# Kernel optimization log

Hardware: AMD Instinct MI355X
Metric: run time of the kernel (lower is better)

## Reference

```python
import jax, jax.numpy as jnp
import numpy as np

TOP_K = 2
B, S, H, I, E = 1, 2048, 1024, 4096, 8


def setup_inputs() -> dict:
    key = jax.random.key(0)
    k1, k2, k3, k4 = jax.random.split(key, 4)
    x = jax.random.normal(k1, (B, S, H), dtype=jnp.float32)
    gate_w = jax.random.normal(k2, (E, H), dtype=jnp.float32)
    w1 = jax.random.normal(k3, (E, I, H), dtype=jnp.float32)
    w2 = jax.random.normal(k4, (E, H, I), dtype=jnp.float32)
    return {"x": x, "gate_w": gate_w, "w1": w1, "w2": w2}


def reference(x, gate_w, w1, w2):
    b, s, h = x.shape
    xf = x.reshape(-1, h)                      # [T, H]
    T = xf.shape[0]
    logits = xf @ gate_w.T                     # [T, E]
    probs = jax.nn.softmax(logits, axis=-1)
    wts, idx = jax.lax.top_k(probs, TOP_K)     # [T, k]
    wts = wts / jnp.sum(wts, axis=-1, keepdims=True)
    # combine[t, e] = routing weight of expert e for token t (0 if not selected)
    combine = jnp.zeros((T, w1.shape[0]), dtype=x.dtype)
    combine = combine.at[jnp.arange(T)[:, None], idx].add(wts)
    # dense dispatch: every expert processes every token, masked/weighted by combine
    hid = jax.nn.silu(jnp.einsum('th,eih->tei', xf, w1))   # [T, E, I]
    y = jnp.einsum('tei,ehi->teh', hid, w2)                # [T, E, H]
    out = jnp.einsum('teh,te->th', y, combine)             # [T, H]
    return out.reshape(b, s, h)
```

## Files before the change

### kernel.cpp

```cpp
#include <hip/hip_runtime.h>
#include <stdint.h>

#define TT 2048
#define HH 1024
#define II 4096
#define EE 8
#define KS 4

typedef __attribute__((ext_vector_type(4))) float floatx4;
typedef __attribute__((ext_vector_type(8))) __bf16 bf16x8;

__device__ __forceinline__ unsigned short f2bf(float f) {
  union { float f; unsigned u; } v; v.f = f;
  return (unsigned short)((v.u + 0x7FFFu + ((v.u >> 16) & 1u)) >> 16);
}

__device__ __forceinline__ void async_ld16(const void* g, void* l) {
  __builtin_amdgcn_global_load_lds(
      (__attribute__((address_space(1))) void*)g,
      (__attribute__((address_space(3))) void*)l, 16, 0, 0);
}

__global__ __launch_bounds__(256) void k_gating(
    const float* __restrict__ x, const float* __restrict__ gw,
    unsigned short* __restrict__ xb, int* __restrict__ sel_e,
    float* __restrict__ sel_w, int* __restrict__ counts) {
  int t = blockIdx.x;
  int tid = threadIdx.x;
  floatx4 xv = ((const floatx4*)(x + (size_t)t * HH))[tid];
  ushort4 xo;
  xo.x = f2bf(xv.x); xo.y = f2bf(xv.y); xo.z = f2bf(xv.z); xo.w = f2bf(xv.w);
  ((ushort4*)(xb + (size_t)t * HH))[tid] = xo;

  float part[EE];
#pragma unroll
  for (int e = 0; e < EE; e++) {
    floatx4 g = ((const floatx4*)(gw + e * HH))[tid];
    part[e] = xv.x * g.x + xv.y * g.y + xv.z * g.z + xv.w * g.w;
  }
#pragma unroll
  for (int e = 0; e < EE; e++) {
    float v = part[e];
#pragma unroll
    for (int off = 32; off > 0; off >>= 1) v += __shfl_down(v, off, 64);
    part[e] = v;
  }
  __shared__ float red[4][EE];
  int wave = tid >> 6;
  if ((tid & 63) == 0) {
#pragma unroll
    for (int e = 0; e < EE; e++) red[wave][e] = part[e];
  }
  __syncthreads();
  if (tid == 0) {
    float lg[EE];
#pragma unroll
    for (int e = 0; e < EE; e++)
      lg[e] = red[0][e] + red[1][e] + red[2][e] + red[3][e];
    int e0 = 0;
#pragma unroll
    for (int e = 1; e < EE; e++) if (lg[e] > lg[e0]) e0 = e;
    int e1 = (e0 == 0) ? 1 : 0;
#pragma unroll
    for (int e = 0; e < EE; e++) if (e != e0 && lg[e] > lg[e1]) e1 = e;
    float w0 = 1.f / (1.f + expf(lg[e1] - lg[e0]));
    sel_e[t * 2] = e0; sel_e[t * 2 + 1] = e1;
    sel_w[t * 2] = w0; sel_w[t * 2 + 1] = 1.f - w0;
    atomicAdd(&counts[e0], 1);
    atomicAdd(&counts[e1], 1);
  }
}

__global__ __launch_bounds__(256) void k_fill(
    const int* __restrict__ counts, const int* __restrict__ sel_e,
    const float* __restrict__ sel_w, int* __restrict__ bases,
    int* __restrict__ row_token, float* __restrict__ row_w,
    int* __restrict__ inv_slot) {
  __shared__ int lb[EE];
  __shared__ int lc[EE];
  int tid = threadIdx.x;
  if (tid == 0) {
    int s = 0;
    for (int e = 0; e < EE; e++) { lb[e] = s; s += counts[e]; }
  }
  if (tid < EE) lc[tid] = 0;
  __syncthreads();
  for (int p = tid; p < TT * 2; p += 256) {
    int e = sel_e[p];
    int slot = lb[e] + atomicAdd(&lc[e], 1);
    row_token[slot] = p >> 1;
    row_w[slot] = sel_w[p];
    inv_slot[p] = slot;
  }
  __syncthreads();
  if (tid < EE) bases[tid] = lb[tid];
}

__global__ __launch_bounds__(256) void k_gemm1(
    const unsigned short* __restrict__ xb,
    const float* __restrict__ w1,
    unsigned short* __restrict__ hid,
    const int* __restrict__ counts, const int* __restrict__ bases,
    const int* __restrict__ row_token) {
  const int e = blockIdx.z;
  const int count = counts[e];
  const int m0 = blockIdx.y * 128;
  if (m0 >= count) return;
  const int n0 = blockIdx.x * 128;
  const int base = bases[e];

  __shared__ __align__(16) unsigned short Smem[128 * 32 * 2];
  unsigned short* As = Smem;
  unsigned short* Bs = Smem + 128 * 32;

  const int tid = threadIdx.x;
  const int lane = tid & 63;
  const int wave = tid >> 6;
  const int wm = (wave & 1) * 64;
  const int wn = (wave >> 1) * 64;
  const int quad = lane >> 4;
  const int l16 = lane & 15;

  const int rA0 = tid >> 2;
  const int rA1 = rA0 + 64;
  const int cc = (tid & 3) * 8;

  int g0 = m0 + rA0; if (g0 > count - 1) g0 = count - 1;
  int g1 = m0 + rA1; if (g1 > count - 1) g1 = count - 1;
  const unsigned short* aS0 = xb + (size_t)row_token[base + g0] * HH + cc;
  const unsigned short* aS1 = xb + (size_t)row_token[base + g1] * HH + cc;
  const float* wp = w1 + (size_t)e * II * HH;
  const float* bp0 = wp + (size_t)(n0 + rA0) * HH + cc;
  const float* bp1 = wp + (size_t)(n0 + rA1) * HH + cc;

  unsigned short* lA0 = As + tid * 8;
  unsigned short* lA1 = As + tid * 8 + 2048;
  unsigned short* lB0 = Bs + tid * 8;
  unsigned short* lB1 = Bs + tid * 8 + 2048;

  const floatx4 fz = {0.f, 0.f, 0.f, 0.f};
  floatx4 acc[4][4];
#pragma unroll
  for (int i = 0; i < 4; i++)
#pragma unroll
    for (int j = 0; j < 4; j++) acc[i][j] = fz;

  floatx4 f0a = *(const floatx4*)(bp0);
  floatx4 f0b = *(const floatx4*)(bp0 + 4);
  floatx4 f1a = *(const floatx4*)(bp1);
  floatx4 f1b = *(const floatx4*)(bp1 + 4);

  for (int k0 = 0; k0 < HH; k0 += 32) {
    bf16x8 wv0, wv1;
#pragma unroll
    for (int j = 0; j < 4; j++) {
      wv0[j] = (__bf16)f0a[j]; wv0[j + 4] = (__bf16)f0b[j];
      wv1[j] = (__bf16)f1a[j]; wv1[j + 4] = (__bf16)f1b[j];
    }
    *(bf16x8*)lB0 = wv0;
    *(bf16x8*)lB1 = wv1;
    async_ld16(aS0 + k0, lA0);
    async_ld16(aS1 + k0, lA1);
    __syncthreads();
    if (k0 + 32 < HH) {
      f0a = *(const floatx4*)(bp0 + k0 + 32);
      f0b = *(const floatx4*)(bp0 + k0 + 36);
      f1a = *(const floatx4*)(bp1 + k0 + 32);
      f1b = *(const floatx4*)(bp1 + k0 + 36);
    }
    bf16x8 af[4], bfr[4];
#pragma unroll
    for (int i = 0; i < 4; i++) {
      af[i]  = *(const bf16x8*)(As + (wm + i * 16 + l16) * 32 + quad * 8);
      bfr[i] = *(const bf16x8*)(Bs + (wn + i * 16 + l16) * 32 + quad * 8);
    }
#pragma unroll
    for (int i = 0; i < 4; i++)
#pragma unroll
      for (int j = 0; j < 4; j++)
        acc[i][j] = __builtin_amdgcn_mfma_f32_16x16x32_bf16(af[i], bfr[j], acc[i][j], 0, 0, 0);
    __syncthreads();
  }

  unsigned short* Sl = Smem + wave * (16 * 72);
#pragma unroll
  for (int i = 0; i < 4; i++) {
#pragma unroll
    for (int r = 0; r < 4; r++) {
      const int row16 = quad * 4 + r;
#pragma unroll
      for (int j = 0; j < 4; j++) {
        float z = acc[i][j][r];
        Sl[row16 * 72 + l16 + 16 * j] = f2bf(z / (1.f + __expf(-z)));
      }
    }
#pragma unroll
    for (int half = 0; half < 2; half++) {
      const int row16 = (lane >> 3) + 8 * half;
      const int m = wm + i * 16 + row16;
      if (m0 + m < count) {
        bf16x8 v = *(const bf16x8*)(Sl + row16 * 72 + (lane & 7) * 8);
        *(bf16x8*)(hid + (size_t)(base + m0 + m) * II + n0 + wn + (lane & 7) * 8) = v;
      }
    }
  }
}

__global__ __launch_bounds__(256) void k_gemm2(
    const unsigned short* __restrict__ hid,
    const float* __restrict__ w2,
    float* __restrict__ yp,
    const int* __restrict__ counts, const int* __restrict__ bases) {
  const int e = blockIdx.z;
  const int count = counts[e];
  const int m0 = blockIdx.y * 128;
  if (m0 >= count) return;
  const int nt = blockIdx.x & 7;
  const int ks = blockIdx.x >> 3;
  const int n0 = nt * 128;
  const int base = bases[e];

  __shared__ __align__(16) unsigned short Smem2[128 * 32 * 2];
  unsigned short* As = Smem2;
  unsigned short* Bs = Smem2 + 128 * 32;

  const int tid = threadIdx.x;
  const int lane = tid & 63;
  const int wave = tid >> 6;
  const int wm = (wave & 1) * 64;
  const int wn = (wave >> 1) * 64;
  const int quad = lane >> 4;
  const int l16 = lane & 15;

  const int rA0 = tid >> 2;
  const int rA1 = rA0 + 64;
  const int cc = (tid & 3) * 8;

  int g0 = m0 + rA0; if (g0 > count - 1) g0 = count - 1;
  int g1 = m0 + rA1; if (g1 > count - 1) g1 = count - 1;
  const unsigned short* aS0 = hid + (size_t)(base + g0) * II + cc;
  const unsigned short* aS1 = hid + (size_t)(base + g1) * II + cc;
  const float* wp = w2 + (size_t)e * HH * II;
  const float* bp0 = wp + (size_t)(n0 + rA0) * II + cc;
  const float* bp1 = wp + (size_t)(n0 + rA1) * II + cc;

  unsigned short* lA0 = As + tid * 8;
  unsigned short* lA1 = As + tid * 8 + 2048;
  unsigned short* lB0 = Bs + tid * 8;
  unsigned short* lB1 = Bs + tid * 8 + 2048;

  const floatx4 fz = {0.f, 0.f, 0.f, 0.f};
  floatx4 acc[4][4];
#pragma unroll
  for (int i = 0; i < 4; i++)
#pragma unroll
    for (int j = 0; j < 4; j++) acc[i][j] = fz;

  const int kbeg = ks * (II / KS);
  const int kend = kbeg + II / KS;

  floatx4 f0a = *(const floatx4*)(bp0 + kbeg);
  floatx4 f0b = *(const floatx4*)(bp0 + kbeg + 4);
  floatx4 f1a = *(const floatx4*)(bp1 + kbeg);
  floatx4 f1b = *(const floatx4*)(bp1 + kbeg + 4);

  for (int k0 = kbeg; k0 < kend; k0 += 32) {
    bf16x8 wv0, wv1;
#pragma unroll
    for (int j = 0; j < 4; j++) {
      wv0[j] = (__bf16)f0a[j]; wv0[j + 4] = (__bf16)f0b[j];
      wv1[j] = (__bf16)f1a[j]; wv1[j + 4] = (__bf16)f1b[j];
    }
    *(bf16x8*)lB0 = wv0;
    *(bf16x8*)lB1 = wv1;
    async_ld16(aS0 + k0, lA0);
    async_ld16(aS1 + k0, lA1);
    __syncthreads();
    if (k0 + 32 < kend) {
      f0a = *(const floatx4*)(bp0 + k0 + 32);
      f0b = *(const floatx4*)(bp0 + k0 + 36);
      f1a = *(const floatx4*)(bp1 + k0 + 32);
      f1b = *(const floatx4*)(bp1 + k0 + 36);
    }
    bf16x8 af[4], bfr[4];
#pragma unroll
    for (int i = 0; i < 4; i++) {
      af[i]  = *(const bf16x8*)(As + (wm + i * 16 + l16) * 32 + quad * 8);
      bfr[i] = *(const bf16x8*)(Bs + (wn + i * 16 + l16) * 32 + quad * 8);
    }
#pragma unroll
    for (int i = 0; i < 4; i++)
#pragma unroll
      for (int j = 0; j < 4; j++)
        acc[i][j] = __builtin_amdgcn_mfma_f32_16x16x32_bf16(af[i], bfr[j], acc[i][j], 0, 0, 0);
    __syncthreads();
  }

#pragma unroll
  for (int i = 0; i < 4; i++) {
#pragma unroll
    for (int r = 0; r < 4; r++) {
      const int m = wm + i * 16 + quad * 4 + r;
      if (m0 + m < count) {
        float* op = yp + ((size_t)ks * (TT * 2) + base + m0 + m) * HH + n0 + wn + l16;
#pragma unroll
        for (int j = 0; j < 4; j++) op[j * 16] = acc[i][j][r];
      }
    }
  }
}

__global__ __launch_bounds__(256) void k_combine(
    const float* __restrict__ yp, const int* __restrict__ inv_slot,
    const float* __restrict__ sel_w, float* __restrict__ out) {
  const int t = blockIdx.x;
  const int tid = threadIdx.x;
  const int s0 = inv_slot[2 * t];
  const int s1 = inv_slot[2 * t + 1];
  const float w0 = sel_w[2 * t];
  const float w1 = sel_w[2 * t + 1];
  floatx4 a = {0.f, 0.f, 0.f, 0.f};
  floatx4 b = {0.f, 0.f, 0.f, 0.f};
#pragma unroll
  for (int ks = 0; ks < KS; ks++) {
    a += ((const floatx4*)(yp + ((size_t)ks * (TT * 2) + s0) * HH))[tid];
    b += ((const floatx4*)(yp + ((size_t)ks * (TT * 2) + s1) * HH))[tid];
  }
  floatx4 v = w0 * a + w1 * b;
  ((floatx4*)(out + (size_t)t * HH))[tid] = v;
}

extern "C" void kernel_launch(void* const* d_in, const int* in_sizes, int n_in,
                              void* d_out, int out_size, void* d_ws, size_t ws_size,
                              hipStream_t stream) {
  const float* x  = (const float*)d_in[0];
  const float* gw = (const float*)d_in[1];
  const float* w1 = (const float*)d_in[2];
  const float* w2 = (const float*)d_in[3];
  float* out = (float*)d_out;

  char* ws = (char*)d_ws;
  size_t off = 0;
  auto take = [&](size_t n) -> char* {
    char* p = ws + off;
    off += (n + 255) & ~(size_t)255;
    return p;
  };
  unsigned short* xb  = (unsigned short*)take((size_t)TT * HH * 2);
  unsigned short* hid = (unsigned short*)take((size_t)TT * 2 * II * 2);
  float* yp = (float*)take((size_t)KS * (TT * 2) * HH * 4);
  int*   counts    = (int*)take(EE * 4);
  int*   bases     = (int*)take(EE * 4);
  int*   row_token = (int*)take((size_t)TT * 2 * 4);
  float* row_w     = (float*)take((size_t)TT * 2 * 4);
  int*   sel_e     = (int*)take((size_t)TT * 2 * 4);
  float* sel_w     = (float*)take((size_t)TT * 2 * 4);
  int*   inv_slot  = (int*)take((size_t)TT * 2 * 4);
  if (off > ws_size) return;

  hipMemsetAsync(counts, 0, EE * 4, stream);

  k_gating<<<TT, 256, 0, stream>>>(x, gw, xb, sel_e, sel_w, counts);
  k_fill<<<1, 256, 0, stream>>>(counts, sel_e, sel_w, bases, row_token, row_w, inv_slot);
  k_gemm1<<<dim3(II / 128, 16, EE), 256, 0, stream>>>(xb, w1, hid, counts, bases, row_token);
  k_gemm2<<<dim3(8 * KS, 16, EE), 256, 0, stream>>>(hid, w2, yp, counts, bases);
  k_combine<<<TT, 256, 0, stream>>>(yp, inv_slot, sel_w, out);
}
```

Measured before the change: 469.8 us.

## Pre-convert weights to bf16 and double-buffer async LDS loads in both GEMMs

Adds a pre-pass kernel that converts w1 and w2 from fp32 to bf16 into workspace on every call. Both expert GEMMs then fetch A and B tiles with global_load_lds into double-buffered, XOR-swizzled shared memory, prefetching the next K step while the MFMAs run. This replaces the per-tile fp32 load and in-register conversion and reduces LDS bank conflicts. In exchange there is a full extra read and write pass over the weights each call, the yp buffer now aliases the w1b workspace, and LDS use per block doubles.

```diff
diff --git a/kernel.cpp b/kernel.cpp
--- a/kernel.cpp
+++ b/kernel.cpp
@@ -6,6 +6,7 @@
 #define II 4096
 #define EE 8
 #define KS 4
+#define KSPAN (II / KS)
 
 typedef __attribute__((ext_vector_type(4))) float floatx4;
 typedef __attribute__((ext_vector_type(8))) __bf16 bf16x8;
@@ -19,6 +20,28 @@
   __builtin_amdgcn_global_load_lds(
       (__attribute__((address_space(1))) void*)g,
       (__attribute__((address_space(3))) void*)l, 16, 0, 0);
+}
+
+#define CFENCE asm volatile("" ::: "memory")
+#define WAIT_VM0 asm volatile("s_waitcnt vmcnt(0)" ::: "memory")
+
+__global__ __launch_bounds__(256) void k_convw(
+    const float* __restrict__ w1, const float* __restrict__ w2,
+    unsigned short* __restrict__ w1b, unsigned short* __restrict__ w2b) {
+  const int N4 = EE * II * HH / 4;
+  int idx = blockIdx.x * 256 + threadIdx.x;
+  const int stride = gridDim.x * 256;
+  for (int i = idx; i < 2 * N4; i += stride) {
+    const float* src;
+    unsigned short* dst;
+    int j;
+    if (i < N4) { src = w1; dst = w1b; j = i; }
+    else        { src = w2; dst = w2b; j = i - N4; }
+    floatx4 a = ((const floatx4*)src)[j];
+    ushort4 o;
+    o.x = f2bf(a.x); o.y = f2bf(a.y); o.z = f2bf(a.z); o.w = f2bf(a.w);
+    ((ushort4*)dst)[j] = o;
+  }
 }
 
 __global__ __launch_bounds__(256) void k_gating(
@@ -98,7 +121,7 @@
 
 __global__ __launch_bounds__(256) void k_gemm1(
     const unsigned short* __restrict__ xb,
-    const float* __restrict__ w1,
+    const unsigned short* __restrict__ w1b,
     unsigned short* __restrict__ hid,
     const int* __restrict__ counts, const int* __restrict__ bases,
     const int* __restrict__ row_token) {
@@ -109,9 +132,11 @@
   const int n0 = blockIdx.x * 128;
   const int base = bases[e];
 
-  __shared__ __align__(16) unsigned short Smem[128 * 32 * 2];
-  unsigned short* As = Smem;
-  unsigned short* Bs = Smem + 128 * 32;
+  __shared__ __align__(16) unsigned short Smem[4 * 4096];
+  unsigned short* const A0b = Smem;
+  unsigned short* const A1b = Smem + 4096;
+  unsigned short* const B0b = Smem + 8192;
+  unsigned short* const B1b = Smem + 12288;
 
   const int tid = threadIdx.x;
   const int lane = tid & 63;
@@ -122,21 +147,26 @@
   const int l16 = lane & 15;
 
   const int rA0 = tid >> 2;
-  const int rA1 = rA0 + 64;
-  const int cc = (tid & 3) * 8;
-
-  int g0 = m0 + rA0; if (g0 > count - 1) g0 = count - 1;
-  int g1 = m0 + rA1; if (g1 > count - 1) g1 = count - 1;
+  const int swz = (tid & 3) ^ ((tid >> 3) & 3);
+  const int cc = swz * 8;
+  const int ldsOff = tid * 8;
+
+  int g0 = m0 + rA0;      if (g0 > count - 1) g0 = count - 1;
+  int g1 = m0 + rA0 + 64; if (g1 > count - 1) g1 = count - 1;
   const unsigned short* aS0 = xb + (size_t)row_token[base + g0] * HH + cc;
   const unsigned short* aS1 = xb + (size_t)row_token[base + g1] * HH + cc;
-  const float* wp = w1 + (size_t)e * II * HH;
-  const float* bp0 = wp + (size_t)(n0 + rA0) * HH + cc;
-  const float* bp1 = wp + (size_t)(n0 + rA1) * HH + cc;
-
-  unsigned short* lA0 = As + tid * 8;
-  unsigned short* lA1 = As + tid * 8 + 2048;
-  unsigned short* lB0 = Bs + tid * 8;
-  unsigned short* lB1 = Bs + tid * 8 + 2048;
+  const unsigned short* wp = w1b + (size_t)e * II * HH;
+  const unsigned short* bS0 = wp + (size_t)(n0 + rA0) * HH + cc;
+  const unsigned short* bS1 = bS0 + (size_t)64 * HH;
+
+  int offA[4], offB[4];
+#pragma unroll
+  for (int i = 0; i < 4; i++) {
+    const int Ra = wm + i * 16 + l16;
+    offA[i] = Ra * 32 + 8 * (quad ^ ((Ra >> 1) & 3));
+    const int Rb = wn + i * 16 + l16;
+    offB[i] = Rb * 32 + 8 * (quad ^ ((Rb >> 1) & 3));
+  }
 
   const floatx4 fz = {0.f, 0.f, 0.f, 0.f};
   floatx4 acc[4][4];
@@ -145,41 +175,41 @@
 #pragma unroll
     for (int j = 0; j < 4; j++) acc[i][j] = fz;
 
-  floatx4 f0a = *(const floatx4*)(bp0);
-  floatx4 f0b = *(const floatx4*)(bp0 + 4);
-  floatx4 f1a = *(const floatx4*)(bp1);
-  floatx4 f1b = *(const floatx4*)(bp1 + 4);
+  async_ld16(aS0, A0b + ldsOff);
+  async_ld16(aS1, A0b + ldsOff + 2048);
+  async_ld16(bS0, B0b + ldsOff);
+  async_ld16(bS1, B0b + ldsOff + 2048);
+  WAIT_VM0;
+  __builtin_amdgcn_s_barrier();
+  CFENCE;
+
+  unsigned short* Ac = A0b; unsigned short* An = A1b;
+  unsigned short* Bc = B0b; unsigned short* Bn = B1b;
 
   for (int k0 = 0; k0 < HH; k0 += 32) {
-    bf16x8 wv0, wv1;
-#pragma unroll
-    for (int j = 0; j < 4; j++) {
-      wv0[j] = (__bf16)f0a[j]; wv0[j + 4] = (__bf16)f0b[j];
-      wv1[j] = (__bf16)f1a[j]; wv1[j + 4] = (__bf16)f1b[j];
-    }
-    *(bf16x8*)lB0 = wv0;
-    *(bf16x8*)lB1 = wv1;
-    async_ld16(aS0 + k0, lA0);
-    async_ld16(aS1 + k0, lA1);
-    __syncthreads();
     if (k0 + 32 < HH) {
-      f0a = *(const floatx4*)(bp0 + k0 + 32);
-      f0b = *(const floatx4*)(bp0 + k0 + 36);
-      f1a = *(const floatx4*)(bp1 + k0 + 32);
-      f1b = *(const floatx4*)(bp1 + k0 + 36);
-    }
+      async_ld16(aS0 + k0 + 32, An + ldsOff);
+      async_ld16(aS1 + k0 + 32, An + ldsOff + 2048);
+      async_ld16(bS0 + k0 + 32, Bn + ldsOff);
+      async_ld16(bS1 + k0 + 32, Bn + ldsOff + 2048);
+    }
+    CFENCE;
     bf16x8 af[4], bfr[4];
 #pragma unroll
     for (int i = 0; i < 4; i++) {
-      af[i]  = *(const bf16x8*)(As + (wm + i * 16 + l16) * 32 + quad * 8);
-      bfr[i] = *(const bf16x8*)(Bs + (wn + i * 16 + l16) * 32 + quad * 8);
+      af[i]  = *(const bf16x8*)(Ac + offA[i]);
+      bfr[i] = *(const bf16x8*)(Bc + offB[i]);
     }
 #pragma unroll
     for (int i = 0; i < 4; i++)
 #pragma unroll
       for (int j = 0; j < 4; j++)
         acc[i][j] = __builtin_amdgcn_mfma_f32_16x16x32_bf16(af[i], bfr[j], acc[i][j], 0, 0, 0);
-    __syncthreads();
+    WAIT_VM0;
+    __builtin_amdgcn_s_barrier();
+    CFENCE;
+    { unsigned short* t = Ac; Ac = An; An = t; }
+    { unsigned short* t = Bc; Bc = Bn; Bn = t; }
   }
 
   unsigned short* Sl = Smem + wave * (16 * 72);
@@ -208,7 +238,7 @@
 
 __global__ __launch_bounds__(256) void k_gemm2(
     const unsigned short* __restrict__ hid,
-    const float* __restrict__ w2,
+    const unsigned short* __restrict__ w2b,
     float* __restrict__ yp,
     const int* __restrict__ counts, const int* __restrict__ bases) {
   const int e = blockIdx.z;
@@ -219,10 +249,13 @@
   const int ks = blockIdx.x >> 3;
   const int n0 = nt * 128;
   const int base = bases[e];
-
-  __shared__ __align__(16) unsigned short Smem2[128 * 32 * 2];
-  unsigned short* As = Smem2;
-  unsigned short* Bs = Smem2 + 128 * 32;
+  const int kbeg = ks * KSPAN;
+
+  __shared__ __align__(16) unsigned short Smem2[4 * 4096];
+  unsigned short* const A0b = Smem2;
+  unsigned short* const A1b = Smem2 + 4096;
+  unsigned short* const B0b = Smem2 + 8192;
+  unsigned short* const B1b = Smem2 + 12288;
 
   const int tid = threadIdx.x;
   const int lane = tid & 63;
@@ -233,21 +266,26 @@
   const int l16 = lane & 15;
 
   const int rA0 = tid >> 2;
-  const int rA1 = rA0 + 64;
-  const int cc = (tid & 3) * 8;
-
-  int g0 = m0 + rA0; if (g0 > count - 1) g0 = count - 1;
-  int g1 = m0 + rA1; if (g1 > count - 1) g1 = count - 1;
-  const unsigned short* aS0 = hid + (size_t)(base + g0) * II + cc;
-  const unsigned short* aS1 = hid + (size_t)(base + g1) * II + cc;
-  const float* wp = w2 + (size_t)e * HH * II;
-  const float* bp0 = wp + (size_t)(n0 + rA0) * II + cc;
-  const float* bp1 = wp + (size_t)(n0 + rA1) * II + cc;
-
-  unsigned short* lA0 = As + tid * 8;
-  unsigned short* lA1 = As + tid * 8 + 2048;
-  unsigned short* lB0 = Bs + tid * 8;
-  unsigned short* lB1 = Bs + tid * 8 + 2048;
+  const int swz = (tid & 3) ^ ((tid >> 3) & 3);
+  const int cc = swz * 8;
+  const int ldsOff = tid * 8;
+
+  int g0 = m0 + rA0;      if (g0 > count - 1) g0 = count - 1;
+  int g1 = m0 + rA0 + 64; if (g1 > count - 1) g1 = count - 1;
+  const unsigned short* aS0 = hid + (size_t)(base + g0) * II + kbeg + cc;
+  const unsigned short* aS1 = hid + (size_t)(base + g1) * II + kbeg + cc;
+  const unsigned short* wp = w2b + (size_t)e * HH * II;
+  const unsigned short* bS0 = wp + (size_t)(n0 + rA0) * II + kbeg + cc;
+  const unsigned short* bS1 = bS0 + (size_t)64 * II;
+
+  int offA[4], offB[4];
+#pragma unroll
+  for (int i = 0; i < 4; i++) {
+    const int Ra = wm + i * 16 + l16;
+    offA[i] = Ra * 32 + 8 * (quad ^ ((Ra >> 1) & 3));
+    const int Rb = wn + i * 16 + l16;
+    offB[i] = Rb * 32 + 8 * (quad ^ ((Rb >> 1) & 3));
+  }
 
   const floatx4 fz = {0.f, 0.f, 0.f, 0.f};
   floatx4 acc[4][4];
@@ -256,44 +294,41 @@
 #pragma unroll
     for (int j = 0; j < 4; j++) acc[i][j] = fz;
 
-  const int kbeg = ks * (II / KS);
-  const int kend = kbeg + II / KS;
-
-  floatx4 f0a = *(const floatx4*)(bp0 + kbeg);
-  floatx4 f0b = *(const floatx4*)(bp0 + kbeg + 4);
-  floatx4 f1a = *(const floatx4*)(bp1 + kbeg);
-  floatx4 f1b = *(const floatx4*)(bp1 + kbeg + 4);
-
-  for (int k0 = kbeg; k0 < kend; k0 += 32) {
-    bf16x8 wv0, wv1;
-#pragma unroll
-    for (int j = 0; j < 4; j++) {
-      wv0[j] = (__bf16)f0a[j]; wv0[j + 4] = (__bf16)f0b[j];
-      wv1[j] = (__bf16)f1a[j]; wv1[j + 4] = (__bf16)f1b[j];
-    }
-    *(bf16x8*)lB0 = wv0;
-    *(bf16x8*)lB1 = wv1;
-    async_ld16(aS0 + k0, lA0);
-    async_ld16(aS1 + k0, lA1);
-    __syncthreads();
-    if (k0 + 32 < kend) {
-      f0a = *(const floatx4*)(bp0 + k0 + 32);
-      f0b = *(const floatx4*)(bp0 + k0 + 36);
-      f1a = *(const floatx4*)(bp1 + k0 + 32);
-      f1b = *(const floatx4*)(bp1 + k0 + 36);
-    }
+  async_ld16(aS0, A0b + ldsOff);
+  async_ld16(aS1, A0b + ldsOff + 2048);
+  async_ld16(bS0, B0b + ldsOff);
+  async_ld16(bS1, B0b + ldsOff + 2048);
+  WAIT_VM0;
+  __builtin_amdgcn_s_barrier();
+  CFENCE;
+
+  unsigned short* Ac = A0b; unsigned short* An = A1b;
+  unsigned short* Bc = B0b; unsigned short* Bn = B1b;
+
+  for (int k0 = 0; k0 < KSPAN; k0 += 32) {
+    if (k0 + 32 < KSPAN) {
+      async_ld16(aS0 + k0 + 32, An + ldsOff);
+      async_ld16(aS1 + k0 + 32, An + ldsOff + 2048);
+      async_ld16(bS0 + k0 + 32, Bn + ldsOff);
+      async_ld16(bS1 + k0 + 32, Bn + ldsOff + 2048);
+    }
+    CFENCE;
     bf16x8 af[4], bfr[4];
 #pragma unroll
     for (int i = 0; i < 4; i++) {
-      af[i]  = *(const bf16x8*)(As + (wm + i * 16 + l16) * 32 + quad * 8);
-      bfr[i] = *(const bf16x8*)(Bs + (wn + i * 16 + l16) * 32 + quad * 8);
+      af[i]  = *(const bf16x8*)(Ac + offA[i]);
+      bfr[i] = *(const bf16x8*)(Bc + offB[i]);
     }
 #pragma unroll
     for (int i = 0; i < 4; i++)
 #pragma unroll
       for (int j = 0; j < 4; j++)
         acc[i][j] = __builtin_amdgcn_mfma_f32_16x16x32_bf16(af[i], bfr[j], acc[i][j], 0, 0, 0);
-    __syncthreads();
+    WAIT_VM0;
+    __builtin_amdgcn_s_barrier();
+    CFENCE;
+    { unsigned short* t = Ac; Ac = An; An = t; }
+    { unsigned short* t = Bc; Bc = Bn; Bn = t; }
   }
 
 #pragma unroll
@@ -348,7 +383,9 @@
   };
   unsigned short* xb  = (unsigned short*)take((size_t)TT * HH * 2);
   unsigned short* hid = (unsigned short*)take((size_t)TT * 2 * II * 2);
-  float* yp = (float*)take((size_t)KS * (TT * 2) * HH * 4);
+  unsigned short* w1b = (unsigned short*)take((size_t)EE * II * HH * 2);
+  float* yp = (float*)w1b;
+  unsigned short* w2b = (unsigned short*)take((size_t)EE * II * HH * 2);
   int*   counts    = (int*)take(EE * 4);
   int*   bases     = (int*)take(EE * 4);
   int*   row_token = (int*)take((size_t)TT * 2 * 4);
@@ -360,9 +397,10 @@
 
   hipMemsetAsync(counts, 0, EE * 4, stream);
 
+  k_convw<<<2048, 256, 0, stream>>>(w1, w2, w1b, w2b);
   k_gating<<<TT, 256, 0, stream>>>(x, gw, xb, sel_e, sel_w, counts);
   k_fill<<<1, 256, 0, stream>>>(counts, sel_e, sel_w, bases, row_token, row_w, inv_slot);
-  k_gemm1<<<dim3(II / 128, 16, EE), 256, 0, stream>>>(xb, w1, hid, counts, bases, row_token);
-  k_gemm2<<<dim3(8 * KS, 16, EE), 256, 0, stream>>>(hid, w2, yp, counts, bases);
+  k_gemm1<<<dim3(II / 128, 16, EE), 256, 0, stream>>>(xb, w1b, hid, counts, bases, row_token);
+  k_gemm2<<<dim3(8 * KS, 16, EE), 256, 0, stream>>>(hid, w2b, yp, counts, bases);
   k_combine<<<TT, 256, 0, stream>>>(yp, inv_slot, sel_w, out);
 }
```

Measured after the change: 502.2 us. +6.9%, slower.

## Triple-buffer LDS with explicit waitcnt pipelining and XOR swizzle in both expert GEMMs

Applied to the files above, without the earlier changes.

Both grouped GEMM kernels move from a single-buffered LDS tile with two barriers per k-step to a three-stage rotating buffer. Global weight loads and async A-tile DMA are issued two steps ahead, and progress is tracked with manual s_waitcnt vmcnt/lgkmcnt plus one barrier per step. The LDS layout gets an XOR swizzle on the k-chunk index to cut bank conflicts on the MFMA fragment reads. This costs three times the LDS and more live registers, and leans on hand-written waitcnt counts being correct.

```diff
diff --git a/kernel.cpp b/kernel.cpp
--- a/kernel.cpp
+++ b/kernel.cpp
@@ -6,6 +6,7 @@
 #define II 4096
 #define EE 8
 #define KS 4
+#define KSPAN (II / KS)
 
 typedef __attribute__((ext_vector_type(4))) float floatx4;
 typedef __attribute__((ext_vector_type(8))) __bf16 bf16x8;
@@ -20,6 +21,10 @@
       (__attribute__((address_space(1))) void*)g,
       (__attribute__((address_space(3))) void*)l, 16, 0, 0);
 }
+
+#define CFENCE asm volatile("" ::: "memory")
+#define WAIT_VM(n) asm volatile("s_waitcnt vmcnt(" #n ")" ::: "memory")
+#define WAIT_LGKM0 asm volatile("s_waitcnt lgkmcnt(0)" ::: "memory")
 
 __global__ __launch_bounds__(256) void k_gating(
     const float* __restrict__ x, const float* __restrict__ gw,
@@ -95,6 +100,53 @@
   __syncthreads();
   if (tid < EE) bases[tid] = lb[tid];
 }
+
+#define ISSUE_B(kt, ra, rb, rc, rd)                         \
+  do {                                                      \
+    ra = *(const floatx4*)(bp0 + (size_t)(kt) * 32);        \
+    rb = *(const floatx4*)(bp0 + (size_t)(kt) * 32 + 4);    \
+    rc = *(const floatx4*)(bp1 + (size_t)(kt) * 32);        \
+    rd = *(const floatx4*)(bp1 + (size_t)(kt) * 32 + 4);    \
+    CFENCE;                                                 \
+  } while (0)
+
+#define DMA_A(kt)                                           \
+  do {                                                      \
+    async_ld16(aS0 + (size_t)(kt) * 32, pA2 + ldsOff);      \
+    async_ld16(aS1 + (size_t)(kt) * 32, pA2 + ldsOff + 2048); \
+    CFENCE;                                                 \
+  } while (0)
+
+#define CVT_WR(ra, rb, rc, rd)                              \
+  do {                                                      \
+    bf16x8 wv0, wv1;                                        \
+    _Pragma("unroll") for (int q = 0; q < 4; q++) {         \
+      wv0[q] = (__bf16)ra[q]; wv0[q + 4] = (__bf16)rb[q];   \
+      wv1[q] = (__bf16)rc[q]; wv1[q + 4] = (__bf16)rd[q];   \
+    }                                                       \
+    *(bf16x8*)(pB1 + ldsB) = wv0;                           \
+    *(bf16x8*)(pB1 + ldsB + 2048) = wv1;                    \
+  } while (0)
+
+#define MFMA_STEP                                           \
+  do {                                                      \
+    bf16x8 af[4], bfr[4];                                   \
+    _Pragma("unroll") for (int i = 0; i < 4; i++) {         \
+      af[i]  = *(const bf16x8*)(pA0 + offA[i]);             \
+      bfr[i] = *(const bf16x8*)(pB0 + offB[i]);             \
+    }                                                       \
+    _Pragma("unroll") for (int i = 0; i < 4; i++)           \
+      _Pragma("unroll") for (int jj = 0; jj < 4; jj++)      \
+        acc[i][jj] = __builtin_amdgcn_mfma_f32_16x16x32_bf16(af[i], bfr[jj], acc[i][jj], 0, 0, 0); \
+  } while (0)
+
+#define ROT3                                                \
+  do {                                                      \
+    unsigned short* t_ = pA0; pA0 = pA1; pA1 = pA2; pA2 = t_; \
+    t_ = pB0; pB0 = pB1; pB1 = pB2; pB2 = t_;               \
+  } while (0)
+
+#define BAR  do { __builtin_amdgcn_s_barrier(); CFENCE; } while (0)
 
 __global__ __launch_bounds__(256) void k_gemm1(
     const unsigned short* __restrict__ xb,
@@ -109,9 +161,7 @@
   const int n0 = blockIdx.x * 128;
   const int base = bases[e];
 
-  __shared__ __align__(16) unsigned short Smem[128 * 32 * 2];
-  unsigned short* As = Smem;
-  unsigned short* Bs = Smem + 128 * 32;
+  __shared__ __align__(16) unsigned short Smem[6 * 4096];
 
   const int tid = threadIdx.x;
   const int lane = tid & 63;
@@ -122,21 +172,28 @@
   const int l16 = lane & 15;
 
   const int rA0 = tid >> 2;
-  const int rA1 = rA0 + 64;
-  const int cc = (tid & 3) * 8;
-
-  int g0 = m0 + rA0; if (g0 > count - 1) g0 = count - 1;
-  int g1 = m0 + rA1; if (g1 > count - 1) g1 = count - 1;
-  const unsigned short* aS0 = xb + (size_t)row_token[base + g0] * HH + cc;
-  const unsigned short* aS1 = xb + (size_t)row_token[base + g1] * HH + cc;
+  const int swz = (tid & 3) ^ ((tid >> 3) & 3);
+  const int ccA = swz * 8;
+  const int ccB = (tid & 3) * 8;
+  const int ldsOff = tid * 8;
+  const int ldsB = rA0 * 32 + swz * 8;
+
+  int g0 = m0 + rA0;      if (g0 > count - 1) g0 = count - 1;
+  int g1 = m0 + rA0 + 64; if (g1 > count - 1) g1 = count - 1;
+  const unsigned short* aS0 = xb + (size_t)row_token[base + g0] * HH + ccA;
+  const unsigned short* aS1 = xb + (size_t)row_token[base + g1] * HH + ccA;
   const float* wp = w1 + (size_t)e * II * HH;
-  const float* bp0 = wp + (size_t)(n0 + rA0) * HH + cc;
-  const float* bp1 = wp + (size_t)(n0 + rA1) * HH + cc;
-
-  unsigned short* lA0 = As + tid * 8;
-  unsigned short* lA1 = As + tid * 8 + 2048;
-  unsigned short* lB0 = Bs + tid * 8;
-  unsigned short* lB1 = Bs + tid * 8 + 2048;
+  const float* bp0 = wp + (size_t)(n0 + rA0) * HH + ccB;
+  const float* bp1 = bp0 + (size_t)64 * HH;
+
+  int offA[4], offB[4];
+#pragma unroll
+  for (int i = 0; i < 4; i++) {
+    const int Ra = wm + i * 16 + l16;
+    offA[i] = Ra * 32 + 8 * (quad ^ ((Ra >> 1) & 3));
+    const int Rb = wn + i * 16 + l16;
+    offB[i] = Rb * 32 + 8 * (quad ^ ((Rb >> 1) & 3));
+  }
 
   const floatx4 fz = {0.f, 0.f, 0.f, 0.f};
   floatx4 acc[4][4];
@@ -145,42 +202,45 @@
 #pragma unroll
     for (int j = 0; j < 4; j++) acc[i][j] = fz;
 
-  floatx4 f0a = *(const floatx4*)(bp0);
-  floatx4 f0b = *(const floatx4*)(bp0 + 4);
-  floatx4 f1a = *(const floatx4*)(bp1);
-  floatx4 f1b = *(const floatx4*)(bp1 + 4);
-
-  for (int k0 = 0; k0 < HH; k0 += 32) {
-    bf16x8 wv0, wv1;
-#pragma unroll
-    for (int j = 0; j < 4; j++) {
-      wv0[j] = (__bf16)f0a[j]; wv0[j + 4] = (__bf16)f0b[j];
-      wv1[j] = (__bf16)f1a[j]; wv1[j + 4] = (__bf16)f1b[j];
+  unsigned short* pA0 = Smem;
+  unsigned short* pA1 = Smem + 4096;
+  unsigned short* pA2 = Smem + 8192;
+  unsigned short* pB0 = Smem + 12288;
+  unsigned short* pB1 = Smem + 16384;
+  unsigned short* pB2 = Smem + 20480;
+
+  floatx4 s0a, s0b, s0c, s0d;
+  floatx4 s1a, s1b, s1c, s1d;
+
+  ISSUE_B(0, s0a, s0b, s0c, s0d);
+  { unsigned short* sv = pA2; pA2 = pA0; DMA_A(0); pA2 = sv; }
+  ISSUE_B(1, s1a, s1b, s1c, s1d);
+  { unsigned short* sv = pA2; pA2 = pA1; DMA_A(1); pA2 = sv; }
+  WAIT_VM(6);
+  { unsigned short* sv = pB1; pB1 = pB0; CVT_WR(s0a, s0b, s0c, s0d); pB1 = sv; }
+  WAIT_LGKM0;
+  BAR;
+
+  for (int j = 0; j < 16; ++j) {
+    const int k = 2 * j;
+    if (j < 15) { ISSUE_B(k + 2, s0a, s0b, s0c, s0d); DMA_A(k + 2); }
+    MFMA_STEP;
+    if (j < 15) { WAIT_VM(6); } else { WAIT_VM(0); }
+    CVT_WR(s1a, s1b, s1c, s1d);
+    WAIT_LGKM0;
+    BAR;
+    ROT3;
+    if (j < 15) { ISSUE_B(k + 3, s1a, s1b, s1c, s1d); DMA_A(k + 3); }
+    MFMA_STEP;
+    if (j < 15) {
+      WAIT_VM(6);
+      CVT_WR(s0a, s0b, s0c, s0d);
+      WAIT_LGKM0;
+      BAR;
+      ROT3;
     }
-    *(bf16x8*)lB0 = wv0;
-    *(bf16x8*)lB1 = wv1;
-    async_ld16(aS0 + k0, lA0);
-    async_ld16(aS1 + k0, lA1);
-    __syncthreads();
-    if (k0 + 32 < HH) {
-      f0a = *(const floatx4*)(bp0 + k0 + 32);
-      f0b = *(const floatx4*)(bp0 + k0 + 36);
-      f1a = *(const floatx4*)(bp1 + k0 + 32);
-      f1b = *(const floatx4*)(bp1 + k0 + 36);
-    }
-    bf16x8 af[4], bfr[4];
-#pragma unroll
-    for (int i = 0; i < 4; i++) {
-      af[i]  = *(const bf16x8*)(As + (wm + i * 16 + l16) * 32 + quad * 8);
-      bfr[i] = *(const bf16x8*)(Bs + (wn + i * 16 + l16) * 32 + quad * 8);
-    }
-#pragma unroll
-    for (int i = 0; i < 4; i++)
-#pragma unroll
-      for (int j = 0; j < 4; j++)
-        acc[i][j] = __builtin_amdgcn_mfma_f32_16x16x32_bf16(af[i], bfr[j], acc[i][j], 0, 0, 0);
-    __syncthreads();
-  }
+  }
+  __syncthreads();
 
   unsigned short* Sl = Smem + wave * (16 * 72);
 #pragma unroll
@@ -203,6 +263,7 @@
         *(bf16x8*)(hid + (size_t)(base + m0 + m) * II + n0 + wn + (lane & 7) * 8) = v;
       }
     }
+    __syncthreads();
   }
 }
 
@@ -219,10 +280,9 @@
   const int ks = blockIdx.x >> 3;
   const int n0 = nt * 128;
   const int base = bases[e];
-
-  __shared__ __align__(16) unsigned short Smem2[128 * 32 * 2];
-  unsigned short* As = Smem2;
-  unsigned short* Bs = Smem2 + 128 * 32;
+  const int kbeg = ks * KSPAN;
+
+  __shared__ __align__(16) unsigned short Smem2[6 * 4096];
 
   const int tid = threadIdx.x;
   const int lane = tid & 63;
@@ -233,21 +293,28 @@
   const int l16 = lane & 15;
 
   const int rA0 = tid >> 2;
-  const int rA1 = rA0 + 64;
-  const int cc = (tid & 3) * 8;
-
-  int g0 = m0 + rA0; if (g0 > count - 1) g0 = count - 1;
-  int g1 = m0 + rA1; if (g1 > count - 1) g1 = count - 1;
-  const unsigned short* aS0 = hid + (size_t)(base + g0) * II + cc;
-  const unsigned short* aS1 = hid + (size_t)(base + g1) * II + cc;
+  const int swz = (tid & 3) ^ ((tid >> 3) & 3);
+  const int ccA = swz * 8;
+  const int ccB = (tid & 3) * 8;
+  const int ldsOff = tid * 8;
+  const int ldsB = rA0 * 32 + swz * 8;
+
+  int g0 = m0 + rA0;      if (g0 > count - 1) g0 = count - 1;
+  int g1 = m0 + rA0 + 64; if (g1 > count - 1) g1 = count - 1;
+  const unsigned short* aS0 = hid + (size_t)(base + g0) * II + kbeg + ccA;
+  const unsigned short* aS1 = hid + (size_t)(base + g1) * II + kbeg + ccA;
   const float* wp = w2 + (size_t)e * HH * II;
-  const float* bp0 = wp + (size_t)(n0 + rA0) * II + cc;
-  const float* bp1 = wp + (size_t)(n0 + rA1) * II + cc;
-
-  unsigned short* lA0 = As + tid * 8;
-  unsigned short* lA1 = As + tid * 8 + 2048;
-  unsigned short* lB0 = Bs + tid * 8;
-  unsigned short* lB1 = Bs + tid * 8 + 2048;
+  const float* bp0 = wp + (size_t)(n0 + rA0) * II + kbeg + ccB;
+  const float* bp1 = bp0 + (size_t)64 * II;
+
+  int offA[4], offB[4];
+#pragma unroll
+  for (int i = 0; i < 4; i++) {
+    const int Ra = wm + i * 16 + l16;
+    offA[i] = Ra * 32 + 8 * (quad ^ ((Ra >> 1) & 3));
+    const int Rb = wn + i * 16 + l16;
+    offB[i] = Rb * 32 + 8 * (quad ^ ((Rb >> 1) & 3));
+  }
 
   const floatx4 fz = {0.f, 0.f, 0.f, 0.f};
   floatx4 acc[4][4];
@@ -256,44 +323,43 @@
 #pragma unroll
     for (int j = 0; j < 4; j++) acc[i][j] = fz;
 
-  const int kbeg = ks * (II / KS);
-  const int kend = kbeg + II / KS;
-
-  floatx4 f0a = *(const floatx4*)(bp0 + kbeg);
-  floatx4 f0b = *(const floatx4*)(bp0 + kbeg + 4);
-  floatx4 f1a = *(const floatx4*)(bp1 + kbeg);
-  floatx4 f1b = *(const floatx4*)(bp1 + kbeg + 4);
-
-  for (int k0 = kbeg; k0 < kend; k0 += 32) {
-    bf16x8 wv0, wv1;
-#pragma unroll
-    for (int j = 0; j < 4; j++) {
-      wv0[j] = (__bf16)f0a[j]; wv0[j + 4] = (__bf16)f0b[j];
-      wv1[j] = (__bf16)f1a[j]; wv1[j + 4] = (__bf16)f1b[j];
+  unsigned short* pA0 = Smem2;
+  unsigned short* pA1 = Smem2 + 4096;
+  unsigned short* pA2 = Smem2 + 8192;
+  unsigned short* pB0 = Smem2 + 12288;
+  unsigned short* pB1 = Smem2 + 16384;
+  unsigned short* pB2 = Smem2 + 20480;
+
+  floatx4 s0a, s0b, s0c, s0d;
+  floatx4 s1a, s1b, s1c, s1d;
+
+  ISSUE_B(0, s0a, s0b, s0c, s0d);
+  { unsigned short* sv = pA2; pA2 = pA0; DMA_A(0); pA2 = sv; }
+  ISSUE_B(1, s1a, s1b, s1c, s1d);
+  { unsigned short* sv = pA2; pA2 = pA1; DMA_A(1); pA2 = sv; }
+  WAIT_VM(6);
+  { unsigned short* sv = pB1; pB1 = pB0; CVT_WR(s0a, s0b, s0c, s0d); pB1 = sv; }
+  WAIT_LGKM0;
+  BAR;
+
+  for (int j = 0; j < 16; ++j) {
+    const int k = 2 * j;
+    if (j < 15) { ISSUE_B(k + 2, s0a, s0b, s0c, s0d); DMA_A(k + 2); }
+    MFMA_STEP;
+    if (j < 15) { WAIT_VM(6); } else { WAIT_VM(0); }
+    CVT_WR(s1a, s1b, s1c, s1d);
+    WAIT_LGKM0;
+    BAR;
+    ROT3;
+    if (j < 15) { ISSUE_B(k + 3, s1a, s1b, s1c, s1d); DMA_A(k + 3); }
+    MFMA_STEP;
+    if (j < 15) {
+      WAIT_VM(6);
+      CVT_WR(s0a, s0b, s0c, s0d);
+      WAIT_LGKM0;
+      BAR;
+      ROT3;
     }
-    *(bf16x8*)lB0 = wv0;
-    *(bf16x8*)lB1 = wv1;
-    async_ld16(aS0 + k0, lA0);
-    async_ld16(aS1 + k0, lA1);
-    __syncthreads();
-    if (k0 + 32 < kend) {
-      f0a = *(const floatx4*)(bp0 + k0 + 32);
-      f0b = *(const floatx4*)(bp0 + k0 + 36);
-      f1a = *(const floatx4*)(bp1 + k0 + 32);
-      f1b = *(const floatx4*)(bp1 + k0 + 36);
-    }
-    bf16x8 af[4], bfr[4];
-#pragma unroll
-    for (int i = 0; i < 4; i++) {
-      af[i]  = *(const bf16x8*)(As + (wm + i * 16 + l16) * 32 + quad * 8);
-      bfr[i] = *(const bf16x8*)(Bs + (wn + i * 16 + l16) * 32 + quad * 8);
-    }
-#pragma unroll
-    for (int i = 0; i < 4; i++)
-#pragma unroll
-      for (int j = 0; j < 4; j++)
-        acc[i][j] = __builtin_amdgcn_mfma_f32_16x16x32_bf16(af[i], bfr[j], acc[i][j], 0, 0, 0);
-    __syncthreads();
   }
 
 #pragma unroll
```

Measured after the change: 483.9 us. 1.03x slower.
